# Kernel optimization log

Hardware: AMD Instinct MI355X
Metric: run time of the kernel (lower is better)

## Reference

```python
import jax, jax.numpy as jnp
import numpy as np

# dims
B, N, D, F, L = 512, 128, 256, 16, 3
EPS = 1e-7
MAX_NORM = 1.0 - 1e-5  # PoincareBall proj boundary (c = 1.0)


def _proj(x):
    """Project points into the open Poincare ball (c=1)."""
    n = jnp.maximum(jnp.linalg.norm(x, axis=-1, keepdims=True), EPS)
    scale = jnp.where(n > MAX_NORM, MAX_NORM / n, 1.0)
    return x * scale


def _expmap0(u):
    """Exponential map at the origin, c=1: tanh(||u||) * u / ||u||."""
    n = jnp.maximum(jnp.linalg.norm(u, axis=-1, keepdims=True), EPS)
    return jnp.tanh(n) * u / n


def _logmap0(x):
    """Log map at the origin, c=1: artanh(||x||) * x / ||x||."""
    n = jnp.maximum(jnp.linalg.norm(x, axis=-1, keepdims=True), EPS)
    return jnp.arctanh(jnp.minimum(n, MAX_NORM)) * x / n


def setup_inputs() -> dict:
    key = jax.random.key(0)
    ks = jax.random.split(key, 6)
    # manifold input points: small tangent vectors -> inside the ball
    x = 0.01 * jax.random.normal(ks[0], (B, N, D), dtype=jnp.float32)
    adj = jax.random.uniform(ks[1], (B, N, N), dtype=jnp.float32)
    node_mask = jnp.ones((B, N, 1), dtype=jnp.float32)
    # per-layer HGC linear weights (tangent-space linear), hidden_dim -> hidden_dim
    Ws = jax.random.normal(ks[2], (L, D, D), dtype=jnp.float32) / np.sqrt(D)
    bs = jnp.zeros((L, D), dtype=jnp.float32)
    # final masked linear: hidden_dim -> max_feat_num
    Wout = jax.random.normal(ks[3], (D, F), dtype=jnp.float32) / np.sqrt(D)
    bout = jnp.zeros((F,), dtype=jnp.float32)
    return {"x": x, "adj": adj, "node_mask": node_mask,
            "Ws": Ws, "bs": bs, "Wout": Wout, "bout": bout}


def reference(x, adj, node_mask, Ws, bs, Wout, bout):
    # HGCN decoder: stack of hyperbolic graph-conv layers on the Poincare ball
    # (logmap0 -> tangent linear -> adjacency aggregation -> ReLU -> expmap0),
    # then logmap0 and a masked linear head.
    h = _proj(x)
    for i in range(L):
        t = _logmap0(h)                                  # [B,N,D] tangent at origin
        t = t @ Ws[i] + bs[i]                            # tangent linear
        t = jnp.einsum('bij,bjd->bid', adj, t)           # sum aggregation, norm factor 1
        t = jax.nn.relu(t)                               # activation in tangent space
        h = _proj(_expmap0(t))                           # back to the manifold
    out_tan = _logmap0(h)                                # manifold.logmap0 decode
    type_pred = (out_tan @ Wout + bout) * node_mask      # [B,N,F]
    return type_pred
```

## Files before the change

### kernel.cpp

```cpp
#include <hip/hip_runtime.h>
#include <hip/hip_bf16.h>
#include <math.h>


typedef _Float16 f16;
typedef f16 f16x8 __attribute__((ext_vector_type(8)));
typedef f16 f16x4 __attribute__((ext_vector_type(4)));
typedef f16 f16x2 __attribute__((ext_vector_type(2)));
typedef __fp16 fp16x2_cv __attribute__((ext_vector_type(2)));
typedef float f32x4 __attribute__((ext_vector_type(4)));

#define NB 512
#define NN 128
#define ND 256
#define NF 16
#define NL 3

#define SDT 264
#define SDV 136

#define EPSV   1e-7f
#define MAXN   0.99999f
#define ATHMAX 6.1030340f

__device__ __forceinline__ f16x4 pack4(float a, float b, float c, float d) {
    fp16x2_cv lo = __builtin_amdgcn_cvt_pkrtz(a, b);
    fp16x2_cv hi = __builtin_amdgcn_cvt_pkrtz(c, d);
    f16x2 lo2, hi2;
    __builtin_memcpy(&lo2, &lo, sizeof(lo2));
    __builtin_memcpy(&hi2, &hi, sizeof(hi2));
    return __builtin_shufflevector(lo2, hi2, 0, 1, 2, 3);
}

__global__ void prep_kernel(const float* __restrict__ Ws,
                            const float* __restrict__ Wout,
                            f16* __restrict__ Wt, f16* __restrict__ WoutT) {
    int idx = blockIdx.x * 256 + threadIdx.x;
    if (idx < NL * ND * ND) {
        int l = idx / (ND * ND);
        int r = idx % (ND * ND);
        int n = r >> 8;
        int k = r & 255;
        Wt[idx] = (f16)Ws[l * ND * ND + k * ND + n];
    }
    if (idx < NF * ND) {
        int f = idx >> 8;
        int k = idx & 255;
        WoutT[idx] = (f16)Wout[k * NF + f];
    }
}

__global__ __launch_bounds__(1024, 4)
void hgcn_kernel(const float* __restrict__ x,
                 const float* __restrict__ adj,
                 const float* __restrict__ node_mask,
                 const f16*  __restrict__ Wt,
                 const float* __restrict__ bs,
                 const f16*  __restrict__ WoutT,
                 const float* __restrict__ bout,
                 float* __restrict__ out) {
    __shared__ __align__(16) f16 sT[NN * SDT];
    __shared__ __align__(16) f16 sV[ND * SDV];
    __shared__ float sRed[16 * 16];

    const int b    = blockIdx.x;
    const int tid  = threadIdx.x;
    const int wave = tid >> 6;
    const int lane = tid & 63;
    const int lg   = lane >> 4;
    const int lc   = lane & 15;

    const f32x4 fzero = {0.f, 0.f, 0.f, 0.f};

    f16x8 adjf[4];
    {
        const float* adjb = adj + (size_t)b * NN * NN;
        #pragma unroll
        for (int ks = 0; ks < 4; ++ks) {
            const float4* ap = (const float4*)(adjb + ((wave >> 1) * 16 + lc) * NN + ks * 32 + lg * 8);
            float4 alo = ap[0], ahi = ap[1];
            f16x4 l4 = pack4(alo.x, alo.y, alo.z, alo.w);
            f16x4 h4 = pack4(ahi.x, ahi.y, ahi.z, ahi.w);
            adjf[ks] = __builtin_shufflevector(l4, h4, 0, 1, 2, 3, 4, 5, 6, 7);
        }
    }

    {
        const float4* xb = (const float4*)(x + (size_t)b * NN * ND);
        #pragma unroll
        for (int r = 0; r < 8; ++r) {
            int row = wave * 8 + r;
            float4 v = xb[row * 64 + lane];
            float ssq = v.x * v.x + v.y * v.y + v.z * v.z + v.w * v.w;
            #pragma unroll
            for (int d = 1; d < 64; d <<= 1) ssq += __shfl_xor(ssq, d);
            float norm = sqrtf(ssq);
            float sc1 = (norm > MAXN) ? (MAXN / norm) : 1.0f;
            float hn  = fmaxf(norm * sc1, EPSV);
            float aa  = fminf(hn, MAXN);
            float ath = 0.5f * __logf((1.0f + aa) / (1.0f - aa));
            float s   = sc1 * ath / hn;
            *(f16x4*)&sT[row * SDT + lane * 4] =
                pack4(v.x * s, v.y * s, v.z * s, v.w * s);
        }
    }
    __syncthreads();

    for (int layer = 0; layer < NL; ++layer) {
        const f16* WtL  = Wt + layer * ND * ND;
        const float bias = bs[layer * ND + wave * 16 + lc];

        f32x4 acc_a[8];
        #pragma unroll
        for (int t = 0; t < 8; ++t) acc_a[t] = fzero;

        #pragma unroll
        for (int ks = 0; ks < 8; ++ks) {
            f16x8 bfr = *(const f16x8*)(WtL + (wave * 16 + lc) * ND + ks * 32 + lg * 8);
            #pragma unroll
            for (int mt = 0; mt < 8; ++mt) {
                f16x8 afr = *(const f16x8*)&sT[(mt * 16 + lc) * SDT + ks * 32 + lg * 8];
                acc_a[mt] = __builtin_amdgcn_mfma_f32_16x16x32_f16(afr, bfr, acc_a[mt], 0, 0, 0);
            }
        }
        #pragma unroll
        for (int mt = 0; mt < 8; ++mt) {
            int n  = wave * 16 + lc;
            int m0 = mt * 16 + lg * 4;
            *(f16x4*)&sV[n * SDV + m0] =
                pack4(acc_a[mt][0] + bias, acc_a[mt][1] + bias,
                      acc_a[mt][2] + bias, acc_a[mt][3] + bias);
        }
        __syncthreads();

        f32x4 acc_b[8];
        #pragma unroll
        for (int t = 0; t < 8; ++t) acc_b[t] = fzero;

        #pragma unroll
        for (int ks = 0; ks < 4; ++ks) {
            #pragma unroll
            for (int nt = 0; nt < 8; ++nt) {
                f16x8 afr = *(const f16x8*)&sV[(((wave & 1) * 8 + nt) * 16 + lc) * SDV + ks * 32 + lg * 8];
                acc_b[nt] = __builtin_amdgcn_mfma_f32_16x16x32_f16(afr, adjf[ks], acc_b[nt], 0, 0, 0);
            }
        }

        float ssq = 0.f;
        #pragma unroll
        for (int t = 0; t < 8; ++t)
            #pragma unroll
            for (int r = 0; r < 4; ++r) {
                float v = fmaxf(acc_b[t][r], 0.0f);
                acc_b[t][r] = v;
                ssq += v * v;
            }
        ssq += __shfl_xor(ssq, 16);
        ssq += __shfl_xor(ssq, 32);
        if (lg == 0) sRed[wave * 16 + lc] = ssq;
        __syncthreads();
        float tot = ssq + sRed[(wave ^ 1) * 16 + lc];
        float nu = sqrtf(tot);
        float scale = (nu > ATHMAX) ? (ATHMAX / nu) : 1.0f;

        #pragma unroll
        for (int nt = 0; nt < 8; ++nt) {
            int i  = (wave >> 1) * 16 + lc;
            int k0 = ((wave & 1) * 8 + nt) * 16 + lg * 4;
            *(f16x4*)&sT[i * SDT + k0] =
                pack4(acc_b[nt][0] * scale, acc_b[nt][1] * scale,
                      acc_b[nt][2] * scale, acc_b[nt][3] * scale);
        }
        __syncthreads();
    }

    if (wave < 8) {
        f32x4 acc = fzero;
        #pragma unroll
        for (int ks = 0; ks < 8; ++ks) {
            f16x8 afr = *(const f16x8*)&sT[(wave * 16 + lc) * SDT + ks * 32 + lg * 8];
            f16x8 bfr = *(const f16x8*)(WoutT + lc * ND + ks * 32 + lg * 8);
            acc = __builtin_amdgcn_mfma_f32_16x16x32_f16(afr, bfr, acc, 0, 0, 0);
        }
        #pragma unroll
        for (int r = 0; r < 4; ++r) {
            int row = wave * 16 + lg * 4 + r;
            float mask = node_mask[b * NN + row];
            out[((size_t)b * NN + row) * NF + lc] = (acc[r] + bout[lc]) * mask;
        }
    }
}

extern "C" void kernel_launch(void* const* d_in, const int* in_sizes, int n_in,
                              void* d_out, int out_size, void* d_ws, size_t ws_size,
                              hipStream_t stream) {
    const float* x    = (const float*)d_in[0];
    const float* adj  = (const float*)d_in[1];
    const float* mask = (const float*)d_in[2];
    const float* Ws   = (const float*)d_in[3];
    const float* bsp  = (const float*)d_in[4];
    const float* Wout = (const float*)d_in[5];
    const float* bout = (const float*)d_in[6];

    f16* Wt    = (f16*)d_ws;
    f16* WoutT = Wt + NL * ND * ND;

    prep_kernel<<<768, 256, 0, stream>>>(Ws, Wout, Wt, WoutT);
    hgcn_kernel<<<NB, 1024, 0, stream>>>(x, adj, mask, Wt, bsp, WoutT, bout,
                                         (float*)d_out);
}
```

Baseline: 78.26 us.

## Switch layer GEMMs to 32x32x16 MFMA tiles with new wave partitioning

Both per-layer GEMMs (tangent linear and adjacency aggregation) move from 16x16x32 MFMA to 32x32x16 MFMA, and the work is split across the 16 waves differently. Each wave now computes a 32x64 tile, which cuts LDS and global fragment loads per FLOP. The row-norm reduction changes to a 4-way partial sum through an enlarged sRed buffer. The larger accumulators raise register pressure under the 1024-thread launch bound.

```diff
diff --git a/kernel.cpp b/kernel.cpp
--- a/kernel.cpp
+++ b/kernel.cpp
@@ -9,6 +9,7 @@
 typedef f16 f16x2 __attribute__((ext_vector_type(2)));
 typedef __fp16 fp16x2_cv __attribute__((ext_vector_type(2)));
 typedef float f32x4 __attribute__((ext_vector_type(4)));
+typedef float f32x16 __attribute__((ext_vector_type(16)));
 
 #define NB 512
 #define NN 128
@@ -61,23 +62,30 @@
                  float* __restrict__ out) {
     __shared__ __align__(16) f16 sT[NN * SDT];
     __shared__ __align__(16) f16 sV[ND * SDV];
-    __shared__ float sRed[16 * 16];
+    __shared__ __align__(16) float sRed[NN * 4];
 
     const int b    = blockIdx.x;
     const int tid  = threadIdx.x;
     const int wave = tid >> 6;
     const int lane = tid & 63;
+    const int l31  = lane & 31;
+    const int hi   = lane >> 5;
     const int lg   = lane >> 4;
     const int lc   = lane & 15;
 
-    const f32x4 fzero = {0.f, 0.f, 0.f, 0.f};
-
-    f16x8 adjf[4];
+    const int mr  = wave >> 2;
+    const int nc2 = wave & 3;
+    const int nr2 = wave >> 2;
+    const int ic  = wave & 3;
+
+    const f32x16 fzero16 = {0.f};
+
+    f16x8 adjf[8];
     {
         const float* adjb = adj + (size_t)b * NN * NN;
         #pragma unroll
-        for (int ks = 0; ks < 4; ++ks) {
-            const float4* ap = (const float4*)(adjb + ((wave >> 1) * 16 + lc) * NN + ks * 32 + lg * 8);
+        for (int ks = 0; ks < 8; ++ks) {
+            const float4* ap = (const float4*)(adjb + (ic * 32 + l31) * NN + ks * 16 + hi * 8);
             float4 alo = ap[0], ahi = ap[1];
             f16x4 l4 = pack4(alo.x, alo.y, alo.z, alo.w);
             f16x4 h4 = pack4(ahi.x, ahi.y, ahi.z, ahi.w);
@@ -107,75 +115,81 @@
     __syncthreads();
 
     for (int layer = 0; layer < NL; ++layer) {
-        const f16* WtL  = Wt + layer * ND * ND;
-        const float bias = bs[layer * ND + wave * 16 + lc];
-
-        f32x4 acc_a[8];
-        #pragma unroll
-        for (int t = 0; t < 8; ++t) acc_a[t] = fzero;
-
+        const f16* WtL = Wt + layer * ND * ND;
+
+        f32x16 acc_a0 = fzero16, acc_a1 = fzero16;
+        #pragma unroll
+        for (int ks = 0; ks < 16; ++ks) {
+            f16x8 afr = *(const f16x8*)&sT[(mr * 32 + l31) * SDT + ks * 16 + hi * 8];
+            f16x8 b0 = *(const f16x8*)(WtL + ((2 * nc2 + 0) * 32 + l31) * ND + ks * 16 + hi * 8);
+            f16x8 b1 = *(const f16x8*)(WtL + ((2 * nc2 + 1) * 32 + l31) * ND + ks * 16 + hi * 8);
+            acc_a0 = __builtin_amdgcn_mfma_f32_32x32x16_f16(afr, b0, acc_a0, 0, 0, 0);
+            acc_a1 = __builtin_amdgcn_mfma_f32_32x32x16_f16(afr, b1, acc_a1, 0, 0, 0);
+        }
+        {
+            int n0 = (2 * nc2 + 0) * 32 + l31;
+            int n1 = (2 * nc2 + 1) * 32 + l31;
+            float bias0 = bs[layer * ND + n0];
+            float bias1 = bs[layer * ND + n1];
+            #pragma unroll
+            for (int g = 0; g < 4; ++g) {
+                int m0 = mr * 32 + 8 * g + 4 * hi;
+                *(f16x4*)&sV[n0 * SDV + m0] =
+                    pack4(acc_a0[4 * g + 0] + bias0, acc_a0[4 * g + 1] + bias0,
+                          acc_a0[4 * g + 2] + bias0, acc_a0[4 * g + 3] + bias0);
+                *(f16x4*)&sV[n1 * SDV + m0] =
+                    pack4(acc_a1[4 * g + 0] + bias1, acc_a1[4 * g + 1] + bias1,
+                          acc_a1[4 * g + 2] + bias1, acc_a1[4 * g + 3] + bias1);
+            }
+        }
+        __syncthreads();
+
+        f32x16 acc_b0 = fzero16, acc_b1 = fzero16;
         #pragma unroll
         for (int ks = 0; ks < 8; ++ks) {
-            f16x8 bfr = *(const f16x8*)(WtL + (wave * 16 + lc) * ND + ks * 32 + lg * 8);
-            #pragma unroll
-            for (int mt = 0; mt < 8; ++mt) {
-                f16x8 afr = *(const f16x8*)&sT[(mt * 16 + lc) * SDT + ks * 32 + lg * 8];
-                acc_a[mt] = __builtin_amdgcn_mfma_f32_16x16x32_f16(afr, bfr, acc_a[mt], 0, 0, 0);
-            }
-        }
-        #pragma unroll
-        for (int mt = 0; mt < 8; ++mt) {
-            int n  = wave * 16 + lc;
-            int m0 = mt * 16 + lg * 4;
-            *(f16x4*)&sV[n * SDV + m0] =
-                pack4(acc_a[mt][0] + bias, acc_a[mt][1] + bias,
-                      acc_a[mt][2] + bias, acc_a[mt][3] + bias);
-        }
+            f16x8 a0 = *(const f16x8*)&sV[((2 * nr2 + 0) * 32 + l31) * SDV + ks * 16 + hi * 8];
+            f16x8 a1 = *(const f16x8*)&sV[((2 * nr2 + 1) * 32 + l31) * SDV + ks * 16 + hi * 8];
+            acc_b0 = __builtin_amdgcn_mfma_f32_32x32x16_f16(a0, adjf[ks], acc_b0, 0, 0, 0);
+            acc_b1 = __builtin_amdgcn_mfma_f32_32x32x16_f16(a1, adjf[ks], acc_b1, 0, 0, 0);
+        }
+
+        float ssq = 0.f;
+        #pragma unroll
+        for (int r = 0; r < 16; ++r) {
+            float v0 = fmaxf(acc_b0[r], 0.0f);
+            float v1 = fmaxf(acc_b1[r], 0.0f);
+            acc_b0[r] = v0;
+            acc_b1[r] = v1;
+            ssq += v0 * v0 + v1 * v1;
+        }
+        ssq += __shfl_xor(ssq, 32);
+        if (lane < 32) sRed[(ic * 32 + l31) * 4 + nr2] = ssq;
         __syncthreads();
 
-        f32x4 acc_b[8];
-        #pragma unroll
-        for (int t = 0; t < 8; ++t) acc_b[t] = fzero;
-
-        #pragma unroll
-        for (int ks = 0; ks < 4; ++ks) {
-            #pragma unroll
-            for (int nt = 0; nt < 8; ++nt) {
-                f16x8 afr = *(const f16x8*)&sV[(((wave & 1) * 8 + nt) * 16 + lc) * SDV + ks * 32 + lg * 8];
-                acc_b[nt] = __builtin_amdgcn_mfma_f32_16x16x32_f16(afr, adjf[ks], acc_b[nt], 0, 0, 0);
-            }
-        }
-
-        float ssq = 0.f;
-        #pragma unroll
-        for (int t = 0; t < 8; ++t)
-            #pragma unroll
-            for (int r = 0; r < 4; ++r) {
-                float v = fmaxf(acc_b[t][r], 0.0f);
-                acc_b[t][r] = v;
-                ssq += v * v;
-            }
-        ssq += __shfl_xor(ssq, 16);
-        ssq += __shfl_xor(ssq, 32);
-        if (lg == 0) sRed[wave * 16 + lc] = ssq;
-        __syncthreads();
-        float tot = ssq + sRed[(wave ^ 1) * 16 + lc];
+        f32x4 p = *(const f32x4*)&sRed[(ic * 32 + l31) * 4];
+        float tot = p[0] + p[1] + p[2] + p[3];
         float nu = sqrtf(tot);
         float scale = (nu > ATHMAX) ? (ATHMAX / nu) : 1.0f;
 
-        #pragma unroll
-        for (int nt = 0; nt < 8; ++nt) {
-            int i  = (wave >> 1) * 16 + lc;
-            int k0 = ((wave & 1) * 8 + nt) * 16 + lg * 4;
-            *(f16x4*)&sT[i * SDT + k0] =
-                pack4(acc_b[nt][0] * scale, acc_b[nt][1] * scale,
-                      acc_b[nt][2] * scale, acc_b[nt][3] * scale);
+        {
+            int i = ic * 32 + l31;
+            #pragma unroll
+            for (int g = 0; g < 4; ++g) {
+                int n0 = (2 * nr2 + 0) * 32 + 8 * g + 4 * hi;
+                int n1 = (2 * nr2 + 1) * 32 + 8 * g + 4 * hi;
+                *(f16x4*)&sT[i * SDT + n0] =
+                    pack4(acc_b0[4 * g + 0] * scale, acc_b0[4 * g + 1] * scale,
+                          acc_b0[4 * g + 2] * scale, acc_b0[4 * g + 3] * scale);
+                *(f16x4*)&sT[i * SDT + n1] =
+                    pack4(acc_b1[4 * g + 0] * scale, acc_b1[4 * g + 1] * scale,
+                          acc_b1[4 * g + 2] * scale, acc_b1[4 * g + 3] * scale);
+            }
         }
         __syncthreads();
     }
 
     if (wave < 8) {
-        f32x4 acc = fzero;
+        f32x4 acc = {0.f, 0.f, 0.f, 0.f};
         #pragma unroll
         for (int ks = 0; ks < 8; ++ks) {
             f16x8 afr = *(const f16x8*)&sT[(wave * 16 + lc) * SDT + ks * 32 + lg * 8];
```

Result: slower. 138.3 us (+76.7%).

## Retile tangent-linear GEMM to 32x32x16 MFMA with prefetched weight fragments

Applied to the files above, without the earlier changes.

The first per-layer GEMM (T @ W) switches from 16x16x32 MFMA tiles, where each wave owned one 16-column strip across all 128 rows, to 32x32x16 MFMA tiles. Each wave now owns a 64x32 output block. All weight fragments for the layer are loaded into registers before the MFMA loop, with a scheduling barrier after the loads. This cuts LDS A-fragment reads per wave and raises operand reuse. The cost is more registers for the 16 prefetched B fragments, which could limit occupancy under launch_bounds(1024,4).

```diff
diff --git a/kernel.cpp b/kernel.cpp
--- a/kernel.cpp
+++ b/kernel.cpp
@@ -9,6 +9,7 @@
 typedef f16 f16x2 __attribute__((ext_vector_type(2)));
 typedef __fp16 fp16x2_cv __attribute__((ext_vector_type(2)));
 typedef float f32x4 __attribute__((ext_vector_type(4)));
+typedef float f32x16 __attribute__((ext_vector_type(16)));
 
 #define NB 512
 #define NN 128
@@ -67,10 +68,15 @@
     const int tid  = threadIdx.x;
     const int wave = tid >> 6;
     const int lane = tid & 63;
+    const int l31  = lane & 31;
+    const int hi   = lane >> 5;
     const int lg   = lane >> 4;
     const int lc   = lane & 15;
 
-    const f32x4 fzero = {0.f, 0.f, 0.f, 0.f};
+    const int mr2 = wave & 1;
+    const int nc  = wave >> 1;
+
+    const f32x16 fzero16 = {0.f};
 
     f16x8 adjf[4];
     {
@@ -107,35 +113,55 @@
     __syncthreads();
 
     for (int layer = 0; layer < NL; ++layer) {
-        const f16* WtL  = Wt + layer * ND * ND;
-        const float bias = bs[layer * ND + wave * 16 + lc];
-
-        f32x4 acc_a[8];
-        #pragma unroll
-        for (int t = 0; t < 8; ++t) acc_a[t] = fzero;
+        const f16* WtL = Wt + layer * ND * ND;
+
+        f32x16 acc_a[2];
+        acc_a[0] = fzero16;
+        acc_a[1] = fzero16;
+
+        const f16* wrow = WtL + (nc * 32 + l31) * ND + hi * 8;
+        f16x8 bf0[8], bf1[8];
+        #pragma unroll
+        for (int k = 0; k < 8; ++k)
+            bf0[k] = *(const f16x8*)(wrow + k * 16);
+        #pragma unroll
+        for (int k = 0; k < 8; ++k)
+            bf1[k] = *(const f16x8*)(wrow + 128 + k * 16);
+        __builtin_amdgcn_sched_barrier(0);
 
         #pragma unroll
         for (int ks = 0; ks < 8; ++ks) {
-            f16x8 bfr = *(const f16x8*)(WtL + (wave * 16 + lc) * ND + ks * 32 + lg * 8);
-            #pragma unroll
-            for (int mt = 0; mt < 8; ++mt) {
-                f16x8 afr = *(const f16x8*)&sT[(mt * 16 + lc) * SDT + ks * 32 + lg * 8];
-                acc_a[mt] = __builtin_amdgcn_mfma_f32_16x16x32_f16(afr, bfr, acc_a[mt], 0, 0, 0);
-            }
-        }
-        #pragma unroll
-        for (int mt = 0; mt < 8; ++mt) {
-            int n  = wave * 16 + lc;
-            int m0 = mt * 16 + lg * 4;
-            *(f16x4*)&sV[n * SDV + m0] =
-                pack4(acc_a[mt][0] + bias, acc_a[mt][1] + bias,
-                      acc_a[mt][2] + bias, acc_a[mt][3] + bias);
+            f16x8 a0 = *(const f16x8*)&sT[(mr2 * 64 +      l31) * SDT + ks * 16 + hi * 8];
+            f16x8 a1 = *(const f16x8*)&sT[(mr2 * 64 + 32 + l31) * SDT + ks * 16 + hi * 8];
+            acc_a[0] = __builtin_amdgcn_mfma_f32_32x32x16_f16(a0, bf0[ks], acc_a[0], 0, 0, 0);
+            acc_a[1] = __builtin_amdgcn_mfma_f32_32x32x16_f16(a1, bf0[ks], acc_a[1], 0, 0, 0);
+        }
+        #pragma unroll
+        for (int ks = 0; ks < 8; ++ks) {
+            f16x8 a0 = *(const f16x8*)&sT[(mr2 * 64 +      l31) * SDT + 128 + ks * 16 + hi * 8];
+            f16x8 a1 = *(const f16x8*)&sT[(mr2 * 64 + 32 + l31) * SDT + 128 + ks * 16 + hi * 8];
+            acc_a[0] = __builtin_amdgcn_mfma_f32_32x32x16_f16(a0, bf1[ks], acc_a[0], 0, 0, 0);
+            acc_a[1] = __builtin_amdgcn_mfma_f32_32x32x16_f16(a1, bf1[ks], acc_a[1], 0, 0, 0);
+        }
+
+        {
+            int n = nc * 32 + l31;
+            float bias = bs[layer * ND + n];
+            #pragma unroll
+            for (int t = 0; t < 2; ++t)
+                #pragma unroll
+                for (int g = 0; g < 4; ++g) {
+                    int m0 = (mr2 * 2 + t) * 32 + 8 * g + 4 * hi;
+                    *(f16x4*)&sV[n * SDV + m0] =
+                        pack4(acc_a[t][4 * g + 0] + bias, acc_a[t][4 * g + 1] + bias,
+                              acc_a[t][4 * g + 2] + bias, acc_a[t][4 * g + 3] + bias);
+                }
         }
         __syncthreads();
 
         f32x4 acc_b[8];
         #pragma unroll
-        for (int t = 0; t < 8; ++t) acc_b[t] = fzero;
+        for (int t = 0; t < 8; ++t) acc_b[t] = (f32x4){0.f, 0.f, 0.f, 0.f};
 
         #pragma unroll
         for (int ks = 0; ks < 4; ++ks) {
@@ -175,7 +201,7 @@
     }
 
     if (wave < 8) {
-        f32x4 acc = fzero;
+        f32x4 acc = {0.f, 0.f, 0.f, 0.f};
         #pragma unroll
         for (int ks = 0; ks < 8; ++ks) {
             f16x8 afr = *(const f16x8*)&sT[(wave * 16 + lc) * SDT + ks * 32 + lg * 8];
```

Result: slower. 99.81 us (+27.5%).
